# Optimization experiments

Measured on AMD Instinct MI355X. Metric: run time of the kernel, lower is better.

## Reference

```python
import jax, jax.numpy as jnp
import numpy as np

N, IN_C, HID, OUT = 100000, 128, 128, 64
E, EP = 500000, 100000


def _glorot(key, shape):
    fan_in, fan_out = shape[0], shape[1]
    s = jnp.sqrt(6.0 / (fan_in + fan_out))
    return jax.random.uniform(key, shape, jnp.float32, -s, s)


def setup_inputs() -> dict:
    key = jax.random.key(0)
    ks = jax.random.split(key, 10)
    x = jax.random.normal(ks[0], (N, IN_C), jnp.float32)
    edge_index = jax.random.randint(ks[1], (2, E), 0, N, jnp.int64)
    pos_edge_index = jax.random.randint(ks[2], (2, EP), 0, N, jnp.int64)
    neg_edge_index = jax.random.randint(ks[3], (2, EP), 0, N, jnp.int64)
    return {
        "x": x,
        "edge_index": edge_index,
        "pos_edge_index": pos_edge_index,
        "neg_edge_index": neg_edge_index,
        "Wl1": _glorot(ks[4], (IN_C, HID)),
        "Wr1": _glorot(ks[5], (IN_C, HID)),
        "b1": jnp.zeros((HID,), jnp.float32),
        "Wl2": _glorot(ks[6], (HID, OUT)),
        "Wr2": _glorot(ks[7], (HID, OUT)),
        "b2": jnp.zeros((OUT,), jnp.float32),
    }


def sage_conv(x, src, dst, Wl, Wr, b):
    # mean aggregation of neighbor features: messages x[src] scattered to dst
    agg = jax.ops.segment_sum(x[src], dst, num_segments=N)  # (N, D)
    deg = jax.ops.segment_sum(jnp.ones((src.shape[0],), x.dtype), dst, num_segments=N)
    mean = agg / jnp.clip(deg, 1.0, None)[:, None]
    return mean @ Wl + x @ Wr + b


def decode_dot(z, ei):
    return (z[ei[0]] * z[ei[1]]).sum(axis=1)  # (E,)


def reference(x, edge_index, pos_edge_index, neg_edge_index, Wl1, Wr1, b1, Wl2, Wr2, b2):
    src, dst = edge_index[0], edge_index[1]
    h = jax.nn.relu(sage_conv(x, src, dst, Wl1, Wr1, b1))  # dropout off (eval)
    z = sage_conv(h, src, dst, Wl2, Wr2, b2)
    return decode_dot(z, pos_edge_index), decode_dot(z, neg_edge_index)
```

## Files before the change

kernel.cpp:

```cpp
#include <hip/hip_runtime.h>

#define N_NODES 100000
#define NE 500000
#define NEP 100000
#define NBLK_SCAN ((N_NODES + 255) / 256)

typedef short bf16x8 __attribute__((ext_vector_type(8)));
typedef float f32x4  __attribute__((ext_vector_type(4)));
typedef ushort ushort8v __attribute__((ext_vector_type(8)));

__device__ inline ushort f2bf(float f) {
    uint u = __builtin_bit_cast(uint, f);
    return (ushort)((u + 0x7FFFu + ((u >> 16) & 1u)) >> 16);
}
__device__ inline float bf2f(ushort h) {
    uint u = ((uint)h) << 16;
    return __builtin_bit_cast(float, u);
}
__device__ inline float bflo(uint v) { return __builtin_bit_cast(float, v << 16); }
__device__ inline float bfhi(uint v) { return __builtin_bit_cast(float, v & 0xFFFF0000u); }

__global__ __launch_bounds__(256) void hist_kernel(
    const int* __restrict__ ei, int* __restrict__ cnt) {
    int e = blockIdx.x * 256 + threadIdx.x;
    if (e >= NE) return;
    atomicAdd(&cnt[ei[NE + e]], 1);
}

__global__ __launch_bounds__(256) void scan1_kernel(
    const int* __restrict__ cnt, int* __restrict__ off, int* __restrict__ sums) {
    __shared__ int buf[256];
    int t = threadIdx.x;
    int i = blockIdx.x * 256 + t;
    int v = (i < N_NODES) ? cnt[i] : 0;
    buf[t] = v;
    __syncthreads();
#pragma unroll
    for (int d = 1; d < 256; d <<= 1) {
        int add = (t >= d) ? buf[t - d] : 0;
        __syncthreads();
        buf[t] += add;
        __syncthreads();
    }
    if (i < N_NODES) off[i] = buf[t] - v;
    if (t == 255) sums[blockIdx.x] = buf[255];
}

__global__ __launch_bounds__(256) void scan23_kernel(
    int* __restrict__ off, int* __restrict__ off2, const int* __restrict__ sums) {
    __shared__ int red[256];
    int bid = blockIdx.x, t = threadIdx.x;
    int v = 0;
    if (t < bid) v += sums[t];
    if (t + 256 < bid) v += sums[t + 256];
    red[t] = v;
    __syncthreads();
#pragma unroll
    for (int d = 128; d > 0; d >>= 1) {
        if (t < d) red[t] += red[t + d];
        __syncthreads();
    }
    int pre = red[0];
    int i = bid * 256 + t;
    if (i < N_NODES) {
        int o = off[i] + pre;
        off[i] = o;
        off2[i] = o;
    }
    if (i == 0) off[N_NODES] = NE;
}

__global__ __launch_bounds__(256) void fill_kernel(
    const int* __restrict__ ei, int* __restrict__ off2, int* __restrict__ srcS) {
    int e = blockIdx.x * 256 + threadIdx.x;
    if (e >= NE) return;
    int src = ei[e];
    int dst = ei[NE + e];
    int pos = atomicAdd(&off2[dst], 1);
    srcS[pos] = src;
}

__global__ __launch_bounds__(256) void prep_kernel(
    const float* __restrict__ x, ushort* __restrict__ xb,
    const float* __restrict__ Wl1, const float* __restrict__ Wr1,
    ushort* __restrict__ b1h,
    const float* __restrict__ Wl2, const float* __restrict__ Wr2,
    ushort* __restrict__ b2h, int* __restrict__ cnt) {
    int b = blockIdx.x;
    if (b < 12500) {
        size_t i = ((size_t)b * 256 + threadIdx.x) * 4;
        float4 v = *reinterpret_cast<const float4*>(x + i);
        ushort4 o;
        o.x = f2bf(v.x); o.y = f2bf(v.y); o.z = f2bf(v.z); o.w = f2bf(v.w);
        *reinterpret_cast<ushort4*>(xb + i) = o;
    } else if (b < 12500 + 128) {
        int gid = (b - 12500) * 256 + threadIdx.x;
        int r = gid & 7, lane = (gid >> 3) & 63, t = (gid >> 9) & 7, ks = gid >> 12;
        int k = ks * 32 + ((lane >> 4) << 3) + r;
        int n = t * 16 + (lane & 15);
        float v = (k < 128) ? Wl1[k * 128 + n] : Wr1[(k - 128) * 128 + n];
        b1h[gid] = f2bf(v);
    } else if (b < 12692) {
        int gid = (b - 12628) * 256 + threadIdx.x;
        int r = gid & 7, lane = (gid >> 3) & 63, t = (gid >> 9) & 7, ks = gid >> 12;
        int k = ks * 32 + ((lane >> 4) << 3) + r;
        int col = t * 16 + (lane & 15);
        float v = (col < 64) ? Wl2[k * 64 + col] : Wr2[k * 64 + (col - 64)];
        b2h[gid] = f2bf(v);
    } else {
        int i = ((b - 12692) * 256 + threadIdx.x) * 4;
        *reinterpret_cast<int4*>(cnt + i) = make_int4(0, 0, 0, 0);
    }
}

__global__ __launch_bounds__(256) void agg_mean_kernel(
    const ushort* __restrict__ xb, const int* __restrict__ off,
    const int* __restrict__ srcS, ushort* __restrict__ meanH) {
    int n = blockIdx.x * 8 + (threadIdx.x >> 5);
    if (n >= N_NODES) return;
    int l = threadIdx.x & 31;
    int s0 = off[n], s1 = off[n + 1];
    float a0 = 0.f, a1 = 0.f, a2 = 0.f, a3 = 0.f;
    int k = s0;
    for (; k + 4 <= s1; k += 4) {
        int sa = srcS[k], sb = srcS[k + 1], sc = srcS[k + 2], sd = srcS[k + 3];
        uint2 va = *(const uint2*)(xb + (size_t)sa * 128 + l * 4);
        uint2 vb = *(const uint2*)(xb + (size_t)sb * 128 + l * 4);
        uint2 vc = *(const uint2*)(xb + (size_t)sc * 128 + l * 4);
        uint2 vd = *(const uint2*)(xb + (size_t)sd * 128 + l * 4);
        a0 += bflo(va.x) + bflo(vb.x) + bflo(vc.x) + bflo(vd.x);
        a1 += bfhi(va.x) + bfhi(vb.x) + bfhi(vc.x) + bfhi(vd.x);
        a2 += bflo(va.y) + bflo(vb.y) + bflo(vc.y) + bflo(vd.y);
        a3 += bfhi(va.y) + bfhi(vb.y) + bfhi(vc.y) + bfhi(vd.y);
    }
    for (; k < s1; ++k) {
        uint2 v = *(const uint2*)(xb + (size_t)srcS[k] * 128 + l * 4);
        a0 += bflo(v.x); a1 += bfhi(v.x);
        a2 += bflo(v.y); a3 += bfhi(v.y);
    }
    float inv = (s1 > s0) ? 1.0f / (float)(s1 - s0) : 0.0f;
    uint2 o;
    o.x = (uint)f2bf(a0 * inv) | ((uint)f2bf(a1 * inv) << 16);
    o.y = (uint)f2bf(a2 * inv) | ((uint)f2bf(a3 * inv) << 16);
    *(uint2*)(meanH + (size_t)n * 128 + l * 4) = o;
}

__global__ __launch_bounds__(512) void mlp_kernel(
    const ushort* __restrict__ meanH, const ushort* __restrict__ xb,
    const ushort* __restrict__ b1h, const float* __restrict__ b1,
    const ushort* __restrict__ b2h,
    ushort* __restrict__ tb, ushort* __restrict__ ub) {
    __shared__ __align__(16) ushort Ws[49152];
    __shared__ __align__(16) ushort hs[8][2048];
    const int tid = threadIdx.x;
    const int w = tid >> 6, lane = tid & 63;
    const int lrow = lane & 15, kg = lane >> 4;
    int wid = blockIdx.x * 8 + w;
    if (wid > N_NODES / 16 - 1) wid = N_NODES / 16 - 1;
    const size_t r0 = (size_t)wid * 16;
    char* hw = (char*)&hs[w][0];
    const f32x4 z4 = {0.f, 0.f, 0.f, 0.f};

    bf16x8 aF[8];
#pragma unroll
    for (int ks = 0; ks < 4; ++ks)
        aF[ks] = *(const bf16x8*)(meanH + (r0 + lrow) * 128 + ks * 32 + kg * 8);
#pragma unroll
    for (int ks = 0; ks < 4; ++ks)
        aF[4 + ks] = *(const bf16x8*)(xb + (r0 + lrow) * 128 + ks * 32 + kg * 8);

    {
        const ushort8v* src1 = (const ushort8v*)b1h;
        const ushort8v* src2 = (const ushort8v*)b2h;
        ushort8v* dst = (ushort8v*)Ws;
#pragma unroll
        for (int i = 0; i < 12; ++i) {
            int j = tid + i * 512;
            dst[j] = (j < 4096) ? src1[j] : src2[j - 4096];
        }
    }
    __syncthreads();

    f32x4 acc[8];
#pragma unroll
    for (int t = 0; t < 8; ++t) acc[t] = z4;
#pragma unroll
    for (int ks = 0; ks < 8; ++ks) {
#pragma unroll
        for (int t = 0; t < 8; ++t) {
            bf16x8 Bh = *(const bf16x8*)(Ws + (ks * 8 + t) * 512 + lane * 8);
            acc[t] = __builtin_amdgcn_mfma_f32_16x16x32_bf16(aF[ks], Bh, acc[t], 0, 0, 0);
        }
    }

#pragma unroll
    for (int t = 0; t < 8; ++t) {
        float bj = b1[t * 16 + lrow];
#pragma unroll
        for (int rg = 0; rg < 4; ++rg) {
            int row = kg * 4 + rg;
            int col2 = (t * 16 + lrow) * 2;
            int byte = row * 256 + (col2 ^ ((row & 7) << 4));
            *(ushort*)(hw + byte) = f2bf(fmaxf(acc[t][rg] + bj, 0.0f));
        }
    }

    bf16x8 hF[4];
#pragma unroll
    for (int ks = 0; ks < 4; ++ks) {
        int byte = lrow * 256 + ((ks * 64 + kg * 16) ^ ((lrow & 7) << 4));
        hF[ks] = *(const bf16x8*)(hw + byte);
    }
    f32x4 acc2[8];
#pragma unroll
    for (int t = 0; t < 8; ++t) acc2[t] = z4;
#pragma unroll
    for (int ks = 0; ks < 4; ++ks) {
#pragma unroll
        for (int t = 0; t < 8; ++t) {
            bf16x8 Bh = *(const bf16x8*)(Ws + 32768 + (ks * 8 + t) * 512 + lane * 8);
            acc2[t] = __builtin_amdgcn_mfma_f32_16x16x32_bf16(hF[ks], Bh, acc2[t], 0, 0, 0);
        }
    }

#pragma unroll
    for (int t = 0; t < 8; ++t) {
#pragma unroll
        for (int rg = 0; rg < 4; ++rg) {
            size_t row = r0 + kg * 4 + rg;
            int col = t * 16 + lrow;
            if (t < 4) tb[row * 64 + col] = f2bf(acc2[t][rg]);
            else       ub[row * 64 + (col - 64)] = f2bf(acc2[t][rg]);
        }
    }
}

__global__ __launch_bounds__(256) void agg_z_kernel(
    const ushort* __restrict__ tb, const ushort* __restrict__ ub,
    const float* __restrict__ b2, const int* __restrict__ off,
    const int* __restrict__ srcS, ushort* __restrict__ zb) {
    int n = blockIdx.x * 32 + (threadIdx.x >> 3);
    if (n >= N_NODES) return;
    int l = threadIdx.x & 7;
    int s0 = off[n], s1 = off[n + 1];
    float a0 = 0.f, a1 = 0.f, a2 = 0.f, a3 = 0.f;
    float a4 = 0.f, a5 = 0.f, a6 = 0.f, a7 = 0.f;
    int k = s0;
#define ACCZ(v)                                                   \
    { a0 += bflo((v).x); a1 += bfhi((v).x);                       \
      a2 += bflo((v).y); a3 += bfhi((v).y);                       \
      a4 += bflo((v).z); a5 += bfhi((v).z);                       \
      a6 += bflo((v).w); a7 += bfhi((v).w); }
    for (; k + 4 <= s1; k += 4) {
        int sa = srcS[k], sb = srcS[k + 1], sc = srcS[k + 2], sd = srcS[k + 3];
        uint4 va = *(const uint4*)(tb + (size_t)sa * 64 + l * 8);
        uint4 vb = *(const uint4*)(tb + (size_t)sb * 64 + l * 8);
        uint4 vc = *(const uint4*)(tb + (size_t)sc * 64 + l * 8);
        uint4 vd = *(const uint4*)(tb + (size_t)sd * 64 + l * 8);
        ACCZ(va) ACCZ(vb) ACCZ(vc) ACCZ(vd)
    }
    for (; k < s1; ++k) {
        uint4 v = *(const uint4*)(tb + (size_t)srcS[k] * 64 + l * 8);
        ACCZ(v)
    }
#undef ACCZ
    float inv = (s1 > s0) ? 1.0f / (float)(s1 - s0) : 0.0f;
    uint4 uu = *(const uint4*)(ub + (size_t)n * 64 + l * 8);
    const float* bp = b2 + l * 8;
    uint4 o;
    o.x = (uint)f2bf(a0 * inv + bflo(uu.x) + bp[0]) | ((uint)f2bf(a1 * inv + bfhi(uu.x) + bp[1]) << 16);
    o.y = (uint)f2bf(a2 * inv + bflo(uu.y) + bp[2]) | ((uint)f2bf(a3 * inv + bfhi(uu.y) + bp[3]) << 16);
    o.z = (uint)f2bf(a4 * inv + bflo(uu.z) + bp[4]) | ((uint)f2bf(a5 * inv + bfhi(uu.z) + bp[5]) << 16);
    o.w = (uint)f2bf(a6 * inv + bflo(uu.w) + bp[6]) | ((uint)f2bf(a7 * inv + bfhi(uu.w) + bp[7]) << 16);
    *(uint4*)(zb + (size_t)n * 64 + l * 8) = o;
}

__global__ __launch_bounds__(256) void decode_kernel(
    const ushort* __restrict__ zb,
    const int* __restrict__ pos, const int* __restrict__ neg,
    float* __restrict__ out) {
    int t = blockIdx.x * 256 + threadIdx.x;
    int g = t >> 3;
    int lane = t & 7;
    if (g >= 2 * NEP) return;
    const int* ei;
    int e;
    float* o;
    if (g < NEP) { ei = pos; e = g; o = out; }
    else         { ei = neg; e = g - NEP; o = out + NEP; }
    int a  = ei[e];
    int bn = ei[NEP + e];
    uint4 va = *reinterpret_cast<const uint4*>(zb + (size_t)a  * 64 + lane * 8);
    uint4 vb = *reinterpret_cast<const uint4*>(zb + (size_t)bn * 64 + lane * 8);
    float s = bflo(va.x) * bflo(vb.x) + bfhi(va.x) * bfhi(vb.x)
            + bflo(va.y) * bflo(vb.y) + bfhi(va.y) * bfhi(vb.y)
            + bflo(va.z) * bflo(vb.z) + bfhi(va.z) * bfhi(vb.z)
            + bflo(va.w) * bflo(vb.w) + bfhi(va.w) * bfhi(vb.w);
    s += __shfl_xor(s, 1);
    s += __shfl_xor(s, 2);
    s += __shfl_xor(s, 4);
    if (lane == 0) o[e] = s;
}

extern "C" void kernel_launch(void* const* d_in, const int* in_sizes, int n_in,
                              void* d_out, int out_size, void* d_ws, size_t ws_size,
                              hipStream_t stream) {
    const float* x    = (const float*)d_in[0];
    const int*   ei   = (const int*)d_in[1];
    const int*   pos  = (const int*)d_in[2];
    const int*   neg  = (const int*)d_in[3];
    const float* Wl1  = (const float*)d_in[4];
    const float* Wr1  = (const float*)d_in[5];
    const float* b1   = (const float*)d_in[6];
    const float* Wl2  = (const float*)d_in[7];
    const float* Wr2  = (const float*)d_in[8];
    const float* b2   = (const float*)d_in[9];
    float* out = (float*)d_out;

    const size_t HALF = (size_t)N_NODES * 128 * 2;
    const size_t QTR  = (size_t)N_NODES * 64 * 2;
    char* ws = (char*)d_ws;
    ushort* xb    = (ushort*)ws;
    ushort* meanH = (ushort*)(ws + HALF);
    ushort* tb    = (ushort*)(ws + 2 * HALF);
    ushort* ub    = (ushort*)(ws + 2 * HALF + QTR);
    ushort* zb    = (ushort*)(ws + 2 * HALF + 2 * QTR);
    int* cnt  = (int*)(ws + 2 * HALF + 3 * QTR);
    int* off  = cnt + N_NODES;
    int* off2 = off + N_NODES + 1;
    int* srcS = off2 + N_NODES;
    int* sums = srcS + NE;
    ushort* b1h = (ushort*)(sums + 512);
    ushort* b2h = b1h + 32768;

    prep_kernel<<<12790, 256, 0, stream>>>(x, xb, Wl1, Wr1, b1h, Wl2, Wr2, b2h, cnt);

    hist_kernel <<<(NE + 255) / 256, 256, 0, stream>>>(ei, cnt);
    scan1_kernel<<<NBLK_SCAN, 256, 0, stream>>>(cnt, off, sums);
    scan23_kernel<<<NBLK_SCAN, 256, 0, stream>>>(off, off2, sums);
    fill_kernel <<<(NE + 255) / 256, 256, 0, stream>>>(ei, off2, srcS);

    agg_mean_kernel<<<N_NODES / 8, 256, 0, stream>>>(xb, off, srcS, meanH);

    mlp_kernel<<<(N_NODES / 16 + 7) / 8, 512, 0, stream>>>(
        meanH, xb, b1h, b1, b2h, tb, ub);

    agg_z_kernel<<<N_NODES / 32 + 1, 256, 0, stream>>>(tb, ub, b2, off, srcS, zb);

    decode_kernel<<<(2 * NEP * 8 + 255) / 256, 256, 0, stream>>>(zb, pos, neg, out);
}
```

Measured before the change: 146.3 us.

## Fuse neighbor mean aggregation into MLP kernel, drop meanH buffer

Removes the separate agg_mean kernel and computes each node's neighbor mean inside the MFMA MLP kernel. Each lane gathers 8-wide bf16 slices of its row's neighbors straight into the A-fragment layout, accumulates in fp32 and converts to bf16 before the matmul. This saves one launch plus the write and reread of the meanH intermediate. In exchange, only the 16 rows of each wave do the gather, with 4 lanes per row loading 16 bytes each, so there is less memory parallelism per byte and more registers in use in the MLP kernel.

After: 148.7 us. About the same (+1.6%).

```diff
diff --git a/kernel.cpp b/kernel.cpp
--- a/kernel.cpp
+++ b/kernel.cpp
@@ -113,40 +113,9 @@
     }
 }
 
-__global__ __launch_bounds__(256) void agg_mean_kernel(
+__global__ __launch_bounds__(512) void mlp_kernel(
     const ushort* __restrict__ xb, const int* __restrict__ off,
-    const int* __restrict__ srcS, ushort* __restrict__ meanH) {
-    int n = blockIdx.x * 8 + (threadIdx.x >> 5);
-    if (n >= N_NODES) return;
-    int l = threadIdx.x & 31;
-    int s0 = off[n], s1 = off[n + 1];
-    float a0 = 0.f, a1 = 0.f, a2 = 0.f, a3 = 0.f;
-    int k = s0;
-    for (; k + 4 <= s1; k += 4) {
-        int sa = srcS[k], sb = srcS[k + 1], sc = srcS[k + 2], sd = srcS[k + 3];
-        uint2 va = *(const uint2*)(xb + (size_t)sa * 128 + l * 4);
-        uint2 vb = *(const uint2*)(xb + (size_t)sb * 128 + l * 4);
-        uint2 vc = *(const uint2*)(xb + (size_t)sc * 128 + l * 4);
-        uint2 vd = *(const uint2*)(xb + (size_t)sd * 128 + l * 4);
-        a0 += bflo(va.x) + bflo(vb.x) + bflo(vc.x) + bflo(vd.x);
-        a1 += bfhi(va.x) + bfhi(vb.x) + bfhi(vc.x) + bfhi(vd.x);
-        a2 += bflo(va.y) + bflo(vb.y) + bflo(vc.y) + bflo(vd.y);
-        a3 += bfhi(va.y) + bfhi(vb.y) + bfhi(vc.y) + bfhi(vd.y);
-    }
-    for (; k < s1; ++k) {
-        uint2 v = *(const uint2*)(xb + (size_t)srcS[k] * 128 + l * 4);
-        a0 += bflo(v.x); a1 += bfhi(v.x);
-        a2 += bflo(v.y); a3 += bfhi(v.y);
-    }
-    float inv = (s1 > s0) ? 1.0f / (float)(s1 - s0) : 0.0f;
-    uint2 o;
-    o.x = (uint)f2bf(a0 * inv) | ((uint)f2bf(a1 * inv) << 16);
-    o.y = (uint)f2bf(a2 * inv) | ((uint)f2bf(a3 * inv) << 16);
-    *(uint2*)(meanH + (size_t)n * 128 + l * 4) = o;
-}
-
-__global__ __launch_bounds__(512) void mlp_kernel(
-    const ushort* __restrict__ meanH, const ushort* __restrict__ xb,
+    const int* __restrict__ srcS,
     const ushort* __restrict__ b1h, const float* __restrict__ b1,
     const ushort* __restrict__ b2h,
     ushort* __restrict__ tb, ushort* __restrict__ ub) {
@@ -161,10 +130,10 @@
     char* hw = (char*)&hs[w][0];
     const f32x4 z4 = {0.f, 0.f, 0.f, 0.f};
 
+    const int n = (int)r0 + lrow;
+    const int s0 = off[n], s1 = off[n + 1];
+
     bf16x8 aF[8];
-#pragma unroll
-    for (int ks = 0; ks < 4; ++ks)
-        aF[ks] = *(const bf16x8*)(meanH + (r0 + lrow) * 128 + ks * 32 + kg * 8);
 #pragma unroll
     for (int ks = 0; ks < 4; ++ks)
         aF[4 + ks] = *(const bf16x8*)(xb + (r0 + lrow) * 128 + ks * 32 + kg * 8);
@@ -177,6 +146,55 @@
         for (int i = 0; i < 12; ++i) {
             int j = tid + i * 512;
             dst[j] = (j < 4096) ? src1[j] : src2[j - 4096];
+        }
+    }
+
+    float ga[4][8];
+#pragma unroll
+    for (int ks = 0; ks < 4; ++ks)
+#pragma unroll
+        for (int j = 0; j < 8; ++j) ga[ks][j] = 0.f;
+#define ACCG(ks, v)                                                       \
+    { ga[ks][0] += bflo((v).x); ga[ks][1] += bfhi((v).x);                 \
+      ga[ks][2] += bflo((v).y); ga[ks][3] += bfhi((v).y);                 \
+      ga[ks][4] += bflo((v).z); ga[ks][5] += bfhi((v).z);                 \
+      ga[ks][6] += bflo((v).w); ga[ks][7] += bfhi((v).w); }
+    {
+        int k = s0;
+        for (; k + 2 <= s1; k += 2) {
+            int sA = srcS[k], sB = srcS[k + 1];
+            const ushort* rA = xb + (size_t)sA * 128 + kg * 8;
+            const ushort* rB = xb + (size_t)sB * 128 + kg * 8;
+            uint4 vA0 = *(const uint4*)(rA);
+            uint4 vA1 = *(const uint4*)(rA + 32);
+            uint4 vA2 = *(const uint4*)(rA + 64);
+            uint4 vA3 = *(const uint4*)(rA + 96);
+            uint4 vB0 = *(const uint4*)(rB);
+            uint4 vB1 = *(const uint4*)(rB + 32);
+            uint4 vB2 = *(const uint4*)(rB + 64);
+            uint4 vB3 = *(const uint4*)(rB + 96);
+            ACCG(0, vA0) ACCG(1, vA1) ACCG(2, vA2) ACCG(3, vA3)
+            ACCG(0, vB0) ACCG(1, vB1) ACCG(2, vB2) ACCG(3, vB3)
+        }
+        if (k < s1) {
+            int sA = srcS[k];
+            const ushort* rA = xb + (size_t)sA * 128 + kg * 8;
+            uint4 vA0 = *(const uint4*)(rA);
+            uint4 vA1 = *(const uint4*)(rA + 32);
+            uint4 vA2 = *(const uint4*)(rA + 64);
+            uint4 vA3 = *(const uint4*)(rA + 96);
+            ACCG(0, vA0) ACCG(1, vA1) ACCG(2, vA2) ACCG(3, vA3)
+        }
+    }
+#undef ACCG
+    {
+        float inv = (s1 > s0) ? 1.0f / (float)(s1 - s0) : 0.0f;
+#pragma unroll
+        for (int ks = 0; ks < 4; ++ks) {
+            bf16x8 f;
+#pragma unroll
+            for (int j = 0; j < 8; ++j) f[j] = (short)f2bf(ga[ks][j] * inv);
+            aF[ks] = f;
         }
     }
     __syncthreads();
@@ -321,7 +339,6 @@
     const size_t QTR  = (size_t)N_NODES * 64 * 2;
     char* ws = (char*)d_ws;
     ushort* xb    = (ushort*)ws;
-    ushort* meanH = (ushort*)(ws + HALF);
     ushort* tb    = (ushort*)(ws + 2 * HALF);
     ushort* ub    = (ushort*)(ws + 2 * HALF + QTR);
     ushort* zb    = (ushort*)(ws + 2 * HALF + 2 * QTR);
@@ -340,10 +357,8 @@
     scan23_kernel<<<NBLK_SCAN, 256, 0, stream>>>(off, off2, sums);
     fill_kernel <<<(NE + 255) / 256, 256, 0, stream>>>(ei, off2, srcS);
 
-    agg_mean_kernel<<<N_NODES / 8, 256, 0, stream>>>(xb, off, srcS, meanH);
-
     mlp_kernel<<<(N_NODES / 16 + 7) / 8, 512, 0, stream>>>(
-        meanH, xb, b1h, b1, b2h, tb, ub);
+        xb, off, srcS, b1h, b1, b2h, tb, ub);
 
     agg_z_kernel<<<N_NODES / 32 + 1, 256, 0, stream>>>(tb, ub, b2, off, srcS, zb);
 
```
